# Optimization experiments

Measured on AMD Instinct MI355X. Metric: run time of the kernel, lower is better.

## Reference

```python
import jax, jax.numpy as jnp
import numpy as np

N, F, E, B, D = 100000, 256, 128, 10000, 32
GAMMA, ZETA = -0.1, 1.1  # hard-concrete stretch params of L0Dense


def setup_inputs() -> dict:
    key = jax.random.key(0)
    ks = jax.random.split(key, 12)
    return {
        "nodes": jax.random.randint(ks[0], (B,), 0, N),
        "neigh_idx": jax.random.randint(ks[1], (B, D), 0, N),
        "neigh_mask": jax.random.bernoulli(ks[2], 0.9, (B, D)),
        "feature": jax.random.normal(ks[3], (N, F), jnp.float32),
        "W": jax.random.normal(ks[4], (F, E), jnp.float32) * 0.05,
        "b": jnp.zeros((E,), jnp.float32),
        "qz_loga": jax.random.normal(ks[5], (F,), jnp.float32),
        "att1_w": jax.random.normal(ks[6], (2 * E, E), jnp.float32) * 0.05,
        "att1_b": jnp.zeros((E,), jnp.float32),
        "att2_w": jax.random.normal(ks[7], (E, E), jnp.float32) * 0.05,
        "att2_b": jnp.zeros((E,), jnp.float32),
        "att3_w": jax.random.normal(ks[8], (E, 1), jnp.float32) * 0.05,
        "att3_b": jnp.zeros((1,), jnp.float32),
    }


def reference(nodes, neigh_idx, neigh_mask, feature, W, b, qz_loga,
              att1_w, att1_b, att2_w, att2_b, att3_w, att3_b):
    # L0Dense, deterministic (eval) hard-concrete gate on input dims
    z = jnp.clip(jax.nn.sigmoid(qz_loga) * (ZETA - GAMMA) + GAMMA, 0.0, 1.0)
    We = W * z[:, None]                                  # [F, E]

    node_feat = feature[nodes] @ We + b                   # [B, E]
    neigh_feat = feature[neigh_idx] @ We + b              # [B, D, E]

    # GraphRec-style attention MLP over (neighbor, center) pairs
    h = jnp.concatenate(
        [neigh_feat, jnp.broadcast_to(node_feat[:, None, :], neigh_feat.shape)],
        axis=-1)                                          # [B, D, 2E]
    h = jax.nn.relu(h @ att1_w + att1_b)
    h = jax.nn.relu(h @ att2_w + att2_b)
    scores = (h @ att3_w + att3_b)[..., 0]                # [B, D]
    scores = jnp.where(neigh_mask, scores, -1e30)
    att = jax.nn.softmax(scores, axis=-1)                 # [B, D]

    agg = jnp.einsum('bd,bde->be', att, neigh_feat)       # weighted sum
    has_neigh = neigh_mask.any(axis=-1, keepdims=True)
    return jnp.where(has_neigh, agg, node_feat)           # n==0 fallback
```

## Files before the change

### kernel.cpp

```cpp
#include <hip/hip_runtime.h>
#include <hip/hip_bf16.h>
#include <math.h>

#define NN 100000
#define FF 256
#define EE 128
#define BB_ 10000
#define DD 32

typedef __attribute__((ext_vector_type(8))) short short8;
typedef __attribute__((ext_vector_type(4))) float f32x4;

__device__ __forceinline__ short f2bf(float f) {
  __hip_bfloat16 h = __float2bfloat16(f);
  union { __hip_bfloat16 h; short s; } u; u.h = h;
  return u.s;
}
__device__ __forceinline__ float bf2f(short s) {
  union { unsigned u; float f; } v;
  v.u = ((unsigned)(unsigned short)s) << 16;
  return v.f;
}

__device__ __forceinline__ void gll16(const float* g, float* lds) {
  __builtin_amdgcn_global_load_lds(
      (const __attribute__((address_space(1))) unsigned int*)g,
      (__attribute__((address_space(3))) unsigned int*)lds, 16, 0, 0);
}

__global__ __launch_bounds__(256) void k_prep(
    const float* __restrict__ W, const float* __restrict__ qz,
    const float* __restrict__ a1w, const float* __restrict__ a2w,
    const float* __restrict__ bb,
    float* __restrict__ Wef32, short* __restrict__ BT2,
    short* __restrict__ a1wTc, short* __restrict__ w2T,
    float* __restrict__ bias2) {
  int i = blockIdx.x * 256 + threadIdx.x;
  if (i < 32768) {
    int f = i >> 7, e = i & 127;
    float g = qz[f];
    float s = 1.0f / (1.0f + expf(-g));
    float z = fminf(fmaxf(s * 1.2f - 0.1f, 0.0f), 1.0f);
    float v = W[f * 128 + e] * z;
    Wef32[f * 128 + e] = v;
    BT2[e * 256 + f] = f2bf(v);
  } else if (i < 49152) {
    int t = i - 32768; int n = t >> 7, k = t & 127;
    a1wTc[n * 128 + k] = f2bf(a1w[(128 + k) * 128 + n]);
  } else if (i < 65536) {
    int t = i - 49152; int n = t >> 7, k = t & 127;
    w2T[n * 128 + k] = f2bf(a2w[k * 128 + n]);
  } else if (i < 65664) {
    bias2[i - 65536] = bb[i - 65536];
  }
}

__global__ __launch_bounds__(256) void k_compose(
    const float* __restrict__ Wef32, const float* __restrict__ a1w,
    const float* __restrict__ a1b, const float* __restrict__ bb,
    short* __restrict__ BT2, float* __restrict__ bias2) {
  const int n = blockIdx.x;
  const int f = threadIdx.x;
  float s = 0.f;
  for (int e = 0; e < 128; ++e)
    s = fmaf(a1w[e * 128 + n], Wef32[f * 128 + e], s);
  BT2[(size_t)(128 + n) * 256 + f] = f2bf(s);
  if (f == 0) {
    float by = a1b[n];
    for (int e = 0; e < 128; ++e) by = fmaf(bb[e], a1w[e * 128 + n], by);
    bias2[128 + n] = by;
  }
}

__global__ __launch_bounds__(256) void k_xy(
    const float* __restrict__ feat, const short* __restrict__ BT2,
    const float* __restrict__ bias2, short* __restrict__ XY, int M) {
  __shared__ float As[2][32 * 256];
  const int tid = threadIdx.x;
  const int wave = tid >> 6, lane = tid & 63;
  const int wn = wave;
  const int l15 = lane & 15, lg = lane >> 4;
  const int NT = M >> 5;
  const int G = gridDim.x;

  short8 bfr[8][4];
#pragma unroll
  for (int ks = 0; ks < 8; ++ks)
#pragma unroll
    for (int j = 0; j < 4; ++j)
      bfr[ks][j] = *(const short8*)(BT2 +
          (size_t)(wn * 64 + j * 16 + l15) * 256 + (ks * 4 + lg) * 8);
  float bv4[4];
#pragma unroll
  for (int j = 0; j < 4; ++j) bv4[j] = bias2[wn * 64 + j * 16 + l15];

  int t = blockIdx.x;
  if (t < NT) {
#pragma unroll
    for (int it = 0; it < 8; ++it) {
      int r = it * 4 + wave;
      gll16(feat + (size_t)(t * 32 + r) * 256 + ((lane ^ (r & 7)) * 4),
            &As[0][r * 256]);
    }
  }

  int cur = 0;
  for (; t < NT; t += G) {
    const int tn = t + G;
    __builtin_amdgcn_s_barrier();
    if (tn < NT) {
#pragma unroll
      for (int it = 0; it < 8; ++it) {
        int r = it * 4 + wave;
        gll16(feat + (size_t)(tn * 32 + r) * 256 + ((lane ^ (r & 7)) * 4),
              &As[cur ^ 1][r * 256]);
      }
      asm volatile("s_waitcnt vmcnt(8)" ::: "memory");
    } else {
      asm volatile("s_waitcnt vmcnt(0)" ::: "memory");
    }
    __builtin_amdgcn_s_barrier();
    __builtin_amdgcn_sched_barrier(0);

    f32x4 acc[2][4];
#pragma unroll
    for (int i = 0; i < 2; ++i)
#pragma unroll
      for (int j = 0; j < 4; ++j) acc[i][j] = (f32x4){0.f, 0.f, 0.f, 0.f};

    const float* Ab = &As[cur][0];
#pragma unroll
    for (int ks = 0; ks < 8; ++ks) {
      const int kg = ks * 4 + lg;
#pragma unroll
      for (int i = 0; i < 2; ++i) {
        const int r = i * 16 + l15;
        const int sw = r & 7;
        const int c0 = (2 * kg) ^ sw;
        const int c1 = (2 * kg + 1) ^ sw;
        float4 flo = *(const float4*)(Ab + r * 256 + c0 * 4);
        float4 fhi = *(const float4*)(Ab + r * 256 + c1 * 4);
        short8 af;
        af[0] = f2bf(flo.x); af[1] = f2bf(flo.y);
        af[2] = f2bf(flo.z); af[3] = f2bf(flo.w);
        af[4] = f2bf(fhi.x); af[5] = f2bf(fhi.y);
        af[6] = f2bf(fhi.z); af[7] = f2bf(fhi.w);
        __builtin_amdgcn_s_setprio(1);
#pragma unroll
        for (int j = 0; j < 4; ++j)
          acc[i][j] = __builtin_amdgcn_mfma_f32_16x16x32_bf16(
              af, bfr[ks][j], acc[i][j], 0, 0, 0);
        __builtin_amdgcn_s_setprio(0);
      }
    }

#pragma unroll
    for (int i = 0; i < 2; ++i) {
#pragma unroll
      for (int r = 0; r < 4; ++r) {
        int row = t * 32 + i * 16 + lg * 4 + r;
#pragma unroll
        for (int j = 0; j < 4; ++j) {
          int col = wn * 64 + j * 16 + l15;
          XY[(size_t)row * 256 + col] = f2bf(acc[i][j][r] + bv4[j]);
        }
      }
    }
    cur ^= 1;
  }
}

template <int K, int LDA, int LDC, bool AF32, bool OUTBF16>
__global__ __launch_bounds__(256) void k_mm(
    const void* __restrict__ Ap, const short* __restrict__ BT,
    const float* __restrict__ bias, const int* __restrict__ idx,
    void* __restrict__ Cp, int M) {
  __shared__ short As[128 * 64];
  __shared__ short Bs[128 * 64];
  const int tid = threadIdx.x;
  const int mb = blockIdx.x * 128;
  const int col0 = blockIdx.y * 128;
  const int wave = tid >> 6, lane = tid & 63;
  const int wr = wave >> 1, wc = wave & 1;
  const int l15 = lane & 15, lg = lane >> 4;

  size_t abase[4];
#pragma unroll
  for (int s = 0; s < 4; ++s) {
    int row = (tid + s * 256) >> 3;
    int grow = mb + row;
    int gr = 0;
    if (grow < M) gr = idx ? idx[grow] : grow;
    abase[s] = (size_t)gr * LDA;
  }

  f32x4 acc[4][4];
#pragma unroll
  for (int i = 0; i < 4; ++i)
#pragma unroll
    for (int j = 0; j < 4; ++j) acc[i][j] = (f32x4){0.f, 0.f, 0.f, 0.f};

  for (int k0 = 0; k0 < K; k0 += 64) {
#pragma unroll
    for (int s = 0; s < 4; ++s) {
      int q = tid + s * 256;
      int row = q >> 3, c = q & 7;
      short8 av;
      if (AF32) {
        const float* ap = (const float*)Ap + abase[s] + k0 + c * 8;
        float4 f0 = *(const float4*)ap;
        float4 f1 = *(const float4*)(ap + 4);
        av[0] = f2bf(f0.x); av[1] = f2bf(f0.y);
        av[2] = f2bf(f0.z); av[3] = f2bf(f0.w);
        av[4] = f2bf(f1.x); av[5] = f2bf(f1.y);
        av[6] = f2bf(f1.z); av[7] = f2bf(f1.w);
      } else {
        av = *(const short8*)((const short*)Ap + abase[s] + k0 + c * 8);
      }
      *(short8*)(As + row * 64 + 8 * (c ^ (row & 7))) = av;
      short8 bv = *(const short8*)(BT + (size_t)(col0 + row) * K + k0 + c * 8);
      *(short8*)(Bs + row * 64 + 8 * (c ^ (row & 7))) = bv;
    }
    __syncthreads();
#pragma unroll
    for (int ks = 0; ks < 2; ++ks) {
      int c = ks * 4 + lg;
      short8 af[4], bfv[4];
#pragma unroll
      for (int i = 0; i < 4; ++i) {
        int r = wr * 64 + i * 16 + l15;
        af[i] = *(short8*)(As + r * 64 + 8 * (c ^ (r & 7)));
        int n = wc * 64 + i * 16 + l15;
        bfv[i] = *(short8*)(Bs + n * 64 + 8 * (c ^ (n & 7)));
      }
#pragma unroll
      for (int i = 0; i < 4; ++i)
#pragma unroll
        for (int j = 0; j < 4; ++j)
          acc[i][j] = __builtin_amdgcn_mfma_f32_16x16x32_bf16(
              af[i], bfv[j], acc[i][j], 0, 0, 0);
    }
    __syncthreads();
  }

  float bv4[4];
#pragma unroll
  for (int j = 0; j < 4; ++j) {
    int col = wc * 64 + j * 16 + l15;
    bv4[j] = bias ? bias[col0 + col] : 0.f;
  }
#pragma unroll
  for (int i = 0; i < 4; ++i) {
#pragma unroll
    for (int r = 0; r < 4; ++r) {
      int row = mb + wr * 64 + i * 16 + lg * 4 + r;
      if (row < M) {
#pragma unroll
        for (int j = 0; j < 4; ++j) {
          int col = wc * 64 + j * 16 + l15;
          float v = acc[i][j][r] + bv4[j];
          if (OUTBF16)
            ((short*)Cp)[(size_t)row * LDC + col0 + col] = f2bf(v);
          else
            ((float*)Cp)[(size_t)row * LDC + col0 + col] = v;
        }
      }
    }
  }
}

__global__ __launch_bounds__(256) void k_attn4(
    const short* __restrict__ XY, const float* __restrict__ P,
    const int* __restrict__ nodes, const int* __restrict__ nidx,
    const int* __restrict__ nmask, const short* __restrict__ w2T,
    const float* __restrict__ b2, const float* __restrict__ w3,
    const float* __restrict__ b3, float* __restrict__ out) {
  __shared__ int ni_s[4][32];
  __shared__ float sc_s[4][32];
  __shared__ float att_s[4][32];
  const int tid = threadIdx.x;
  const int wave = tid >> 6, lane = tid & 63;
  const int b = blockIdx.x * 4 + wave;
  const int l15 = lane & 15, lg = lane >> 4;

  if (lane < 32) ni_s[wave][lane] = nidx[b * DD + lane];

  const int m = nmask[(size_t)b * DD + (lane & 31)];
  const int nid0 = ni_s[wave][l15];
  const int nid1 = ni_s[wave][16 + l15];
  const short* yr0 = XY + (size_t)nid0 * 256 + 128;
  const short* yr1 = XY + (size_t)nid1 * 256 + 128;
  short8 y0v[4], y1v[4];
#pragma unroll
  for (int ks = 0; ks < 4; ++ks) {
    const int k0 = ks * 32 + lg * 8;
    y0v[ks] = *(const short8*)(yr0 + k0);
    y1v[ks] = *(const short8*)(yr1 + k0);
  }
  unsigned xv[32];
#pragma unroll
  for (int d = 0; d < 32; ++d)
    xv[d] = *(const unsigned*)(XY + (size_t)ni_s[wave][d] * 256 + 2 * lane);

  const float* pr = P + (size_t)b * EE;

  f32x4 acc[2][8];
#pragma unroll
  for (int i = 0; i < 2; ++i)
#pragma unroll
    for (int j = 0; j < 8; ++j) acc[i][j] = (f32x4){0.f, 0.f, 0.f, 0.f};

#pragma unroll
  for (int ks = 0; ks < 4; ++ks) {
    const int k0 = ks * 32 + lg * 8;
    float4 pa = *(const float4*)(pr + k0);
    float4 pb = *(const float4*)(pr + k0 + 4);
    float pf[8] = {pa.x, pa.y, pa.z, pa.w, pb.x, pb.y, pb.z, pb.w};
    short8 a0, a1;
#pragma unroll
    for (int e = 0; e < 8; ++e) {
      a0[e] = f2bf(fmaxf(bf2f(y0v[ks][e]) + pf[e], 0.f));
      a1[e] = f2bf(fmaxf(bf2f(y1v[ks][e]) + pf[e], 0.f));
    }
    short8 bfv[8];
#pragma unroll
    for (int j = 0; j < 8; ++j)
      bfv[j] = *(const short8*)(w2T + (size_t)(j * 16 + l15) * EE + k0);
    __builtin_amdgcn_s_setprio(1);
#pragma unroll
    for (int j = 0; j < 8; ++j) {
      acc[0][j] = __builtin_amdgcn_mfma_f32_16x16x32_bf16(a0, bfv[j],
                                                          acc[0][j], 0, 0, 0);
      acc[1][j] = __builtin_amdgcn_mfma_f32_16x16x32_bf16(a1, bfv[j],
                                                          acc[1][j], 0, 0, 0);
    }
    __builtin_amdgcn_s_setprio(0);
  }

  float b2v[8], w3v[8];
#pragma unroll
  for (int j = 0; j < 8; ++j) {
    int col = j * 16 + l15;
    b2v[j] = b2[col];
    w3v[j] = w3[col];
  }
  float part[2][4];
#pragma unroll
  for (int i = 0; i < 2; ++i)
#pragma unroll
    for (int r = 0; r < 4; ++r) {
      float s = 0.f;
#pragma unroll
      for (int j = 0; j < 8; ++j)
        s += fmaxf(acc[i][j][r] + b2v[j], 0.f) * w3v[j];
      part[i][r] = s;
    }
#pragma unroll
  for (int off = 1; off <= 8; off <<= 1) {
#pragma unroll
    for (int i = 0; i < 2; ++i)
#pragma unroll
      for (int r = 0; r < 4; ++r) part[i][r] += __shfl_xor(part[i][r], off);
  }
  if (l15 == 0) {
#pragma unroll
    for (int i = 0; i < 2; ++i)
#pragma unroll
      for (int r = 0; r < 4; ++r)
        sc_s[wave][i * 16 + lg * 4 + r] = part[i][r];
  }

  const int row = lane & 31;
  float s = sc_s[wave][row] + b3[0];
  if (!m) s = -1e30f;
  float mx = s;
#pragma unroll
  for (int off = 1; off <= 16; off <<= 1) mx = fmaxf(mx, __shfl_xor(mx, off));
  float e = expf(s - mx);
  float sum = e;
#pragma unroll
  for (int off = 1; off <= 16; off <<= 1) sum += __shfl_xor(sum, off);
  if (lane < 32) att_s[wave][row] = e / sum;
  const bool has = (__ballot(m != 0) != 0ull);

  float a0 = 0.f, a1 = 0.f;
  if (has) {
#pragma unroll
    for (int d = 0; d < 32; ++d) {
      float a = att_s[wave][d];
      a0 += a * bf2f((short)(xv[d] & 0xffffu));
      a1 += a * bf2f((short)(xv[d] >> 16));
    }
  } else {
    const short* xr = XY + (size_t)nodes[b] * 256;
    unsigned x2 = *(const unsigned*)(xr + 2 * lane);
    a0 = bf2f((short)(x2 & 0xffffu));
    a1 = bf2f((short)(x2 >> 16));
  }
  *(float2*)(out + (size_t)b * EE + 2 * lane) = make_float2(a0, a1);
}

extern "C" void kernel_launch(void* const* d_in, const int* in_sizes, int n_in,
                              void* d_out, int out_size, void* d_ws,
                              size_t ws_size, hipStream_t stream) {
  const int* nodes = (const int*)d_in[0];
  const int* nidx = (const int*)d_in[1];
  const int* nmask = (const int*)d_in[2];
  const float* feature = (const float*)d_in[3];
  const float* W = (const float*)d_in[4];
  const float* bb = (const float*)d_in[5];
  const float* qz = (const float*)d_in[6];
  const float* a1w = (const float*)d_in[7];
  const float* a1b = (const float*)d_in[8];
  const float* a2w = (const float*)d_in[9];
  const float* a2b = (const float*)d_in[10];
  const float* a3w = (const float*)d_in[11];
  const float* a3b = (const float*)d_in[12];
  float* out = (float*)d_out;

  char* ws = (char*)d_ws;
  short* BT2   = (short*)(ws);
  float* Wef32 = (float*)(ws + 131072);
  short* a1wTc = (short*)(ws + 262144);
  short* w2T   = (short*)(ws + 294912);
  float* bias2 = (float*)(ws + 327680);
  short* XYb   = (short*)(ws + 524288);
  float* Pv    = (float*)(ws + 524288 + 51200000);

  k_prep<<<257, 256, 0, stream>>>(W, qz, a1w, a2w, bb, Wef32, BT2, a1wTc, w2T,
                                  bias2);
  k_compose<<<128, 256, 0, stream>>>(Wef32, a1w, a1b, bb, BT2, bias2);
  k_xy<<<512, 256, 0, stream>>>(feature, BT2, bias2, XYb, NN);
  k_mm<128, 256, 128, false, false><<<dim3((BB_ + 127) / 128, 1), 256, 0,
                                      stream>>>(XYb, a1wTc, nullptr, nodes, Pv,
                                                BB_);
  k_attn4<<<BB_ / 4, 256, 0, stream>>>(XYb, Pv, nodes, nidx, nmask, w2T, a2b,
                                       a3w, a3b, out);
}
```

Baseline: 117.9 us.

## Stage neighbor X rows in LDS with 16-byte loads and split MFMA columns

The attention kernel now loads each neighbor's X half-row with 16-byte vector loads into a per-wave LDS buffer, replacing 32 scattered 4-byte loads held in registers. The aggregation step then reads those rows from LDS. The layer-2 MFMA is split into two 64-column groups with the bias/ReLU/w3 reduction done per group, which roughly halves the live accumulator registers and should help occupancy. The cost is 32 KB of LDS per block, which may limit how many blocks fit on a CU.

```diff
diff --git a/kernel.cpp b/kernel.cpp
--- a/kernel.cpp
+++ b/kernel.cpp
@@ -269,25 +269,29 @@
   }
 }
 
-__global__ __launch_bounds__(256) void k_attn4(
+__global__ __launch_bounds__(256) void k_attn5(
     const short* __restrict__ XY, const float* __restrict__ P,
     const int* __restrict__ nodes, const int* __restrict__ nidx,
     const int* __restrict__ nmask, const short* __restrict__ w2T,
     const float* __restrict__ b2, const float* __restrict__ w3,
     const float* __restrict__ b3, float* __restrict__ out) {
-  __shared__ int ni_s[4][32];
+  __shared__ short xs[4][32 * 128];
   __shared__ float sc_s[4][32];
   __shared__ float att_s[4][32];
   const int tid = threadIdx.x;
   const int wave = tid >> 6, lane = tid & 63;
   const int b = blockIdx.x * 4 + wave;
   const int l15 = lane & 15, lg = lane >> 4;
-
-  if (lane < 32) ni_s[wave][lane] = nidx[b * DD + lane];
+  const int* nb = nidx + b * DD;
 
   const int m = nmask[(size_t)b * DD + (lane & 31)];
-  const int nid0 = ni_s[wave][l15];
-  const int nid1 = ni_s[wave][16 + l15];
+
+  short8 xtmp[8];
+#pragma unroll
+  for (int it = 0; it < 8; ++it)
+    xtmp[it] = *(const short8*)(XY + (size_t)nb[it * 4 + lg] * 256 + l15 * 8);
+  const int nid0 = nb[l15];
+  const int nid1 = nb[16 + l15];
   const short* yr0 = XY + (size_t)nid0 * 256 + 128;
   const short* yr1 = XY + (size_t)nid1 * 256 + 128;
   short8 y0v[4], y1v[4];
@@ -297,77 +301,89 @@
     y0v[ks] = *(const short8*)(yr0 + k0);
     y1v[ks] = *(const short8*)(yr1 + k0);
   }
-  unsigned xv[32];
-#pragma unroll
-  for (int d = 0; d < 32; ++d)
-    xv[d] = *(const unsigned*)(XY + (size_t)ni_s[wave][d] * 256 + 2 * lane);
-
   const float* pr = P + (size_t)b * EE;
-
-  f32x4 acc[2][8];
+  float4 pv[8];
+#pragma unroll
+  for (int q = 0; q < 4; ++q) {
+    const int k0 = q * 32 + lg * 8;
+    pv[2 * q] = *(const float4*)(pr + k0);
+    pv[2 * q + 1] = *(const float4*)(pr + k0 + 4);
+  }
+
+#pragma unroll
+  for (int it = 0; it < 8; ++it)
+    *(short8*)&xs[wave][(it * 4 + lg) * 128 + l15 * 8] = xtmp[it];
+
+  short8 a0[4], a1[4];
+#pragma unroll
+  for (int ks = 0; ks < 4; ++ks) {
+    float pf[8] = {pv[2 * ks].x, pv[2 * ks].y, pv[2 * ks].z, pv[2 * ks].w,
+                   pv[2 * ks + 1].x, pv[2 * ks + 1].y, pv[2 * ks + 1].z,
+                   pv[2 * ks + 1].w};
+#pragma unroll
+    for (int e = 0; e < 8; ++e) {
+      a0[ks][e] = f2bf(fmaxf(bf2f(y0v[ks][e]) + pf[e], 0.f));
+      a1[ks][e] = f2bf(fmaxf(bf2f(y1v[ks][e]) + pf[e], 0.f));
+    }
+  }
+
+  float sp[2][4];
 #pragma unroll
   for (int i = 0; i < 2; ++i)
 #pragma unroll
-    for (int j = 0; j < 8; ++j) acc[i][j] = (f32x4){0.f, 0.f, 0.f, 0.f};
-
-#pragma unroll
-  for (int ks = 0; ks < 4; ++ks) {
-    const int k0 = ks * 32 + lg * 8;
-    float4 pa = *(const float4*)(pr + k0);
-    float4 pb = *(const float4*)(pr + k0 + 4);
-    float pf[8] = {pa.x, pa.y, pa.z, pa.w, pb.x, pb.y, pb.z, pb.w};
-    short8 a0, a1;
-#pragma unroll
-    for (int e = 0; e < 8; ++e) {
-      a0[e] = f2bf(fmaxf(bf2f(y0v[ks][e]) + pf[e], 0.f));
-      a1[e] = f2bf(fmaxf(bf2f(y1v[ks][e]) + pf[e], 0.f));
-    }
-    short8 bfv[8];
-#pragma unroll
-    for (int j = 0; j < 8; ++j)
-      bfv[j] = *(const short8*)(w2T + (size_t)(j * 16 + l15) * EE + k0);
-    __builtin_amdgcn_s_setprio(1);
-#pragma unroll
-    for (int j = 0; j < 8; ++j) {
-      acc[0][j] = __builtin_amdgcn_mfma_f32_16x16x32_bf16(a0, bfv[j],
-                                                          acc[0][j], 0, 0, 0);
-      acc[1][j] = __builtin_amdgcn_mfma_f32_16x16x32_bf16(a1, bfv[j],
-                                                          acc[1][j], 0, 0, 0);
-    }
-    __builtin_amdgcn_s_setprio(0);
-  }
-
-  float b2v[8], w3v[8];
-#pragma unroll
-  for (int j = 0; j < 8; ++j) {
-    int col = j * 16 + l15;
-    b2v[j] = b2[col];
-    w3v[j] = w3[col];
-  }
-  float part[2][4];
-#pragma unroll
-  for (int i = 0; i < 2; ++i)
-#pragma unroll
-    for (int r = 0; r < 4; ++r) {
-      float s = 0.f;
-#pragma unroll
-      for (int j = 0; j < 8; ++j)
-        s += fmaxf(acc[i][j][r] + b2v[j], 0.f) * w3v[j];
-      part[i][r] = s;
-    }
+    for (int r = 0; r < 4; ++r) sp[i][r] = 0.f;
+
+#pragma unroll
+  for (int cg = 0; cg < 2; ++cg) {
+    f32x4 acc[2][4];
+#pragma unroll
+    for (int i = 0; i < 2; ++i)
+#pragma unroll
+      for (int j = 0; j < 4; ++j) acc[i][j] = (f32x4){0.f, 0.f, 0.f, 0.f};
+#pragma unroll
+    for (int ks = 0; ks < 4; ++ks) {
+      const int k0 = ks * 32 + lg * 8;
+      short8 bfv[4];
+#pragma unroll
+      for (int j = 0; j < 4; ++j)
+        bfv[j] = *(const short8*)(w2T +
+            (size_t)(cg * 64 + j * 16 + l15) * EE + k0);
+      __builtin_amdgcn_s_setprio(1);
+#pragma unroll
+      for (int j = 0; j < 4; ++j) {
+        acc[0][j] = __builtin_amdgcn_mfma_f32_16x16x32_bf16(a0[ks], bfv[j],
+                                                            acc[0][j], 0, 0, 0);
+        acc[1][j] = __builtin_amdgcn_mfma_f32_16x16x32_bf16(a1[ks], bfv[j],
+                                                            acc[1][j], 0, 0, 0);
+      }
+      __builtin_amdgcn_s_setprio(0);
+    }
+#pragma unroll
+    for (int j = 0; j < 4; ++j) {
+      const int col = cg * 64 + j * 16 + l15;
+      const float b2v = b2[col];
+      const float w3v = w3[col];
+#pragma unroll
+      for (int i = 0; i < 2; ++i)
+#pragma unroll
+        for (int r = 0; r < 4; ++r)
+          sp[i][r] += fmaxf(acc[i][j][r] + b2v, 0.f) * w3v;
+    }
+  }
+
 #pragma unroll
   for (int off = 1; off <= 8; off <<= 1) {
 #pragma unroll
     for (int i = 0; i < 2; ++i)
 #pragma unroll
-      for (int r = 0; r < 4; ++r) part[i][r] += __shfl_xor(part[i][r], off);
+      for (int r = 0; r < 4; ++r) sp[i][r] += __shfl_xor(sp[i][r], off);
   }
   if (l15 == 0) {
 #pragma unroll
     for (int i = 0; i < 2; ++i)
 #pragma unroll
       for (int r = 0; r < 4; ++r)
-        sc_s[wave][i * 16 + lg * 4 + r] = part[i][r];
+        sc_s[wave][i * 16 + lg * 4 + r] = sp[i][r];
   }
 
   const int row = lane & 31;
@@ -383,21 +399,22 @@
   if (lane < 32) att_s[wave][row] = e / sum;
   const bool has = (__ballot(m != 0) != 0ull);
 
-  float a0 = 0.f, a1 = 0.f;
+  float a0f = 0.f, a1f = 0.f;
   if (has) {
 #pragma unroll
     for (int d = 0; d < 32; ++d) {
-      float a = att_s[wave][d];
-      a0 += a * bf2f((short)(xv[d] & 0xffffu));
-      a1 += a * bf2f((short)(xv[d] >> 16));
+      const float a = att_s[wave][d];
+      const unsigned xdw = *(const unsigned*)&xs[wave][d * 128 + 2 * lane];
+      a0f += a * bf2f((short)(xdw & 0xffffu));
+      a1f += a * bf2f((short)(xdw >> 16));
     }
   } else {
     const short* xr = XY + (size_t)nodes[b] * 256;
     unsigned x2 = *(const unsigned*)(xr + 2 * lane);
-    a0 = bf2f((short)(x2 & 0xffffu));
-    a1 = bf2f((short)(x2 >> 16));
-  }
-  *(float2*)(out + (size_t)b * EE + 2 * lane) = make_float2(a0, a1);
+    a0f = bf2f((short)(x2 & 0xffffu));
+    a1f = bf2f((short)(x2 >> 16));
+  }
+  *(float2*)(out + (size_t)b * EE + 2 * lane) = make_float2(a0f, a1f);
 }
 
 extern "C" void kernel_launch(void* const* d_in, const int* in_sizes, int n_in,
@@ -434,6 +451,6 @@
   k_mm<128, 256, 128, false, false><<<dim3((BB_ + 127) / 128, 1), 256, 0,
                                       stream>>>(XYb, a1wTc, nullptr, nodes, Pv,
                                                 BB_);
-  k_attn4<<<BB_ / 4, 256, 0, stream>>>(XYb, Pv, nodes, nidx, nmask, w2T, a2b,
+  k_attn5<<<BB_ / 4, 256, 0, stream>>>(XYb, Pv, nodes, nidx, nmask, w2T, a2b,
                                        a3w, a3b, out);
 }
```

Result: slower. 125.0 us (+6.0%).
